# Optimization experiments

Hardware: AMD Instinct MI355X
Metric: run time of the kernel (lower is better)

## Reference

```python
import jax, jax.numpy as jnp
import numpy as np

N_NODES = 50000
N_EDGES = 640000
D_IN, D_HID, D_OUT = 128, 256, 2


def setup_inputs() -> dict:
    key = jax.random.key(0)
    ks = jax.random.split(key, 8)
    node_features = jax.random.normal(ks[0], (N_NODES, D_IN), dtype=jnp.float32)
    src = jax.random.randint(ks[1], (N_EDGES,), 0, N_NODES)
    dst = jax.random.randint(ks[2], (N_EDGES,), 0, N_NODES)
    s_in = 1.0 / np.sqrt(D_IN)
    s_hid = 1.0 / np.sqrt(D_HID)
    return {
        "node_features": node_features,
        "src": src,
        "dst": dst,
        "W1_self": jax.random.normal(ks[3], (D_IN, D_HID), dtype=jnp.float32) * s_in,
        "W1_neigh": jax.random.normal(ks[4], (D_IN, D_HID), dtype=jnp.float32) * s_in,
        "b1": jnp.zeros((D_HID,), dtype=jnp.float32),
        "W2_self": jax.random.normal(ks[5], (D_HID, D_OUT), dtype=jnp.float32) * s_hid,
        "W2_neigh": jax.random.normal(ks[6], (D_HID, D_OUT), dtype=jnp.float32) * s_hid,
        "b2": jnp.zeros((D_OUT,), dtype=jnp.float32),
    }


def _sage_mean(x, src, dst, W_self, W_neigh, b, n_nodes):
    # gather source-node features along edges, mean-reduce into destinations
    msg = x[src]                                                  # [E, D]
    agg = jax.ops.segment_sum(msg, dst, num_segments=n_nodes)     # [N, D]
    deg = jax.ops.segment_sum(jnp.ones((src.shape[0], 1), x.dtype), dst,
                              num_segments=n_nodes)               # [N, 1]
    h_neigh = agg / jnp.maximum(deg, 1.0)
    return x @ W_self + h_neigh @ W_neigh + b


def reference(node_features, src, dst, W1_self, W1_neigh, b1, W2_self, W2_neigh, b2):
    h = _sage_mean(node_features, src, dst, W1_self, W1_neigh, b1, N_NODES)
    h = jax.nn.relu(h)
    logits = _sage_mean(h, src, dst, W2_self, W2_neigh, b2, N_NODES)
    return logits
```

## Files before the change

### kernel.cpp

```cpp
#include <hip/hip_runtime.h>

#define D_IN 128
#define D_HID 256
#define CH 1024
#define MPAD 50048

typedef short bf16x8 __attribute__((ext_vector_type(8)));
typedef float f32x4 __attribute__((ext_vector_type(4)));
typedef float f32x16 __attribute__((ext_vector_type(16)));
typedef unsigned short ushort8 __attribute__((ext_vector_type(8)));

#define AS1 __attribute__((address_space(1)))
#define AS3 __attribute__((address_space(3)))

__device__ __forceinline__ unsigned short f2bf_rne(float x) {
  unsigned int u = __float_as_uint(x);
  unsigned int r = (u + 0x7FFFu + ((u >> 16) & 1u)) >> 16;
  return (unsigned short)r;
}
__device__ __forceinline__ float bf2f(unsigned short b) {
  return __uint_as_float(((unsigned int)b) << 16);
}

__global__ void k_hist(const int* __restrict__ dst, int* __restrict__ deg, int E) {
  int e = blockIdx.x * blockDim.x + threadIdx.x;
  if (e < E) atomicAdd(&deg[dst[e]], 1);
}

__global__ __launch_bounds__(256) void k_csum(const int* __restrict__ deg,
                                              int* __restrict__ csum, int n) {
  __shared__ int ws[4];
  int t = threadIdx.x, lane = t & 63, w = t >> 6;
  int base = blockIdx.x * CH + t * 4;
  int s = 0;
  #pragma unroll
  for (int j = 0; j < 4; ++j) { int i = base + j; s += (i < n) ? deg[i] : 0; }
  #pragma unroll
  for (int off = 32; off > 0; off >>= 1) s += __shfl_down(s, off, 64);
  if (lane == 0) ws[w] = s;
  __syncthreads();
  if (t == 0) csum[blockIdx.x] = ws[0] + ws[1] + ws[2] + ws[3];
}

__global__ void k_coff(const int* __restrict__ csum, int* __restrict__ coff, int nb) {
  int lane = threadIdx.x & 63;
  int v = (lane < nb) ? csum[lane] : 0;
  int x = v;
  #pragma unroll
  for (int off = 1; off < 64; off <<= 1) {
    int u = __shfl_up(x, off, 64);
    if (lane >= off) x += u;
  }
  if (lane < nb) coff[lane] = x - v;
}

__global__ __launch_bounds__(256) void k_scanw(const int* __restrict__ deg,
                                               const int* __restrict__ coff,
                                               int* __restrict__ rs, int n) {
  __shared__ int ws[4];
  int t = threadIdx.x, lane = t & 63, w = t >> 6;
  int base = blockIdx.x * CH + t * 4;
  int d[4];
  #pragma unroll
  for (int j = 0; j < 4; ++j) { int i = base + j; d[j] = (i < n) ? deg[i] : 0; }
  int tt = d[0] + d[1] + d[2] + d[3];
  int x = tt;
  #pragma unroll
  for (int off = 1; off < 64; off <<= 1) {
    int u = __shfl_up(x, off, 64);
    if (lane >= off) x += u;
  }
  if (lane == 63) ws[w] = x;
  __syncthreads();
  if (t == 0) { int s = 0;
    #pragma unroll
    for (int j = 0; j < 4; ++j) { int tmp = ws[j]; ws[j] = s; s += tmp; } }
  __syncthreads();
  int excl = ws[w] + (x - tt) + coff[blockIdx.x];
  #pragma unroll
  for (int j = 0; j < 4; ++j) {
    int i = base + j;
    excl += d[j];
    if (i < n) rs[i + 1] = excl;
  }
  if (blockIdx.x == 0 && t == 0) rs[0] = 0;
}

__global__ void k_scatter(const int* __restrict__ src, const int* __restrict__ dst,
                          const int* __restrict__ rs, int* __restrict__ cursor,
                          int* __restrict__ esrc, int E) {
  int e = blockIdx.x * blockDim.x + threadIdx.x;
  if (e < E) {
    int d = dst[e];
    int pos = rs[d] + atomicAdd(&cursor[d], 1);
    esrc[pos] = src[e];
  }
}

__global__ __launch_bounds__(256) void k_convW(const float* __restrict__ W1s,
                                               const float* __restrict__ W1n,
                                               unsigned short* __restrict__ Bth,
                                               unsigned short* __restrict__ Btl) {
  int k = blockIdx.x;
  int col = threadIdx.x;
  float w = (k < 128) ? W1s[(size_t)k * D_HID + col]
                      : W1n[(size_t)(k - 128) * D_HID + col];
  unsigned short hi = f2bf_rne(w);
  unsigned short lo = f2bf_rne(w - bf2f(hi));
  Bth[(size_t)col * 256 + k] = hi;
  Btl[(size_t)col * 256 + k] = lo;
}

__global__ void k_agg1(const float* __restrict__ X, const int* __restrict__ rs,
                       const int* __restrict__ esrc,
                       unsigned short* __restrict__ Mh,
                       unsigned short* __restrict__ Ml, int n) {
  int wid = (blockIdx.x * blockDim.x + threadIdx.x) >> 6;
  int lane = threadIdx.x & 63;
  if (wid >= n) return;
  int s0 = rs[wid], s1 = rs[wid + 1];
  float ax0 = 0.f, ay0 = 0.f, ax1 = 0.f, ay1 = 0.f;
  int e = s0;
  for (; e + 3 < s1; e += 4) {
    int i0 = esrc[e + 0], i1 = esrc[e + 1], i2 = esrc[e + 2], i3 = esrc[e + 3];
    float2 v0 = *(const float2*)(X + (size_t)i0 * D_IN + lane * 2);
    float2 v1 = *(const float2*)(X + (size_t)i1 * D_IN + lane * 2);
    float2 v2 = *(const float2*)(X + (size_t)i2 * D_IN + lane * 2);
    float2 v3 = *(const float2*)(X + (size_t)i3 * D_IN + lane * 2);
    ax0 += v0.x; ay0 += v0.y;
    ax1 += v1.x; ay1 += v1.y;
    ax0 += v2.x; ay0 += v2.y;
    ax1 += v3.x; ay1 += v3.y;
  }
  for (; e < s1; ++e) {
    int s = esrc[e];
    float2 v = *(const float2*)(X + (size_t)s * D_IN + lane * 2);
    ax0 += v.x; ay0 += v.y;
  }
  int d = s1 - s0;
  float inv = 1.0f / (float)(d > 1 ? d : 1);
  float mx = (ax0 + ax1) * inv, my = (ay0 + ay1) * inv;
  unsigned short hx = f2bf_rne(mx), hy = f2bf_rne(my);
  unsigned short lx = f2bf_rne(mx - bf2f(hx)), ly = f2bf_rne(my - bf2f(hy));
  *(ushort2*)(Mh + (size_t)wid * 128 + lane * 2) = make_ushort2(hx, hy);
  *(ushort2*)(Ml + (size_t)wid * 128 + lane * 2) = make_ushort2(lx, ly);
}

__global__ __launch_bounds__(256, 3) void k_gemm1(
    const float* __restrict__ X,
    const unsigned short* __restrict__ Mh, const unsigned short* __restrict__ Ml,
    const unsigned short* __restrict__ Bth, const unsigned short* __restrict__ Btl,
    const float* __restrict__ b1, const float* __restrict__ W2s,
    const float* __restrict__ W2n, float* __restrict__ SP, int n) {
  __shared__ __align__(16) unsigned short sA[2][2][2][512];
  __shared__ __align__(16) unsigned short sB[8][2][2][512];

  const int tid = threadIdx.x;
  const int w = tid >> 6;
  const int l = tid & 63;
  const int wm = w & 1, wn = w >> 1;
  const int r32 = l & 31;
  const int kh = l >> 5;
  const int m0 = blockIdx.x * 64;

  f32x16 acc[4];
  #pragma unroll
  for (int q = 0; q < 4; ++q) acc[q] = (f32x16)0.f;

  const int sm = w & 1, sk = w >> 1;
  const int arow = m0 + sm * 32 + r32;
  const int xrow = (arow < n) ? arow : (n - 1);

  for (int ks = 0; ks < 8; ++ks) {
    const int kt = ks * 32;
    if (kt < 128) {
      const float* src = X + (size_t)xrow * D_IN + kt + sk * 16 + kh * 8;
      float4 u0 = *(const float4*)(src);
      float4 u1 = *(const float4*)(src + 4);
      float v[8] = {u0.x, u0.y, u0.z, u0.w, u1.x, u1.y, u1.z, u1.w};
      ushort8 hh, ll;
      #pragma unroll
      for (int i = 0; i < 8; ++i) {
        unsigned short h = f2bf_rne(v[i]);
        hh[i] = h;
        ll[i] = f2bf_rne(v[i] - bf2f(h));
      }
      *(ushort8*)(&sA[sm][sk][0][l * 8]) = hh;
      *(ushort8*)(&sA[sm][sk][1][l * 8]) = ll;
    } else {
      const unsigned short* mh = Mh + (size_t)arow * 128 + (kt - 128) + sk * 16 + kh * 8;
      const unsigned short* ml = Ml + (size_t)arow * 128 + (kt - 128) + sk * 16 + kh * 8;
      __builtin_amdgcn_global_load_lds((AS1 const void*)mh, (AS3 void*)&sA[sm][sk][0][0], 16, 0, 0);
      __builtin_amdgcn_global_load_lds((AS1 const void*)ml, (AS3 void*)&sA[sm][sk][1][0], 16, 0, 0);
    }
    #pragma unroll
    for (int q = 0; q < 2; ++q) {
      int ct = w * 2 + q;
      #pragma unroll
      for (int kstep = 0; kstep < 2; ++kstep) {
        const unsigned short* bh = Bth + (size_t)(ct * 32 + r32) * 256 + kt + kstep * 16 + kh * 8;
        const unsigned short* bl = Btl + (size_t)(ct * 32 + r32) * 256 + kt + kstep * 16 + kh * 8;
        __builtin_amdgcn_global_load_lds((AS1 const void*)bh, (AS3 void*)&sB[ct][kstep][0][0], 16, 0, 0);
        __builtin_amdgcn_global_load_lds((AS1 const void*)bl, (AS3 void*)&sB[ct][kstep][1][0], 16, 0, 0);
      }
    }
    __syncthreads();

    #pragma unroll
    for (int kstep = 0; kstep < 2; ++kstep) {
      bf16x8 ah = *(const bf16x8*)(&sA[wm][kstep][0][l * 8]);
      bf16x8 al = *(const bf16x8*)(&sA[wm][kstep][1][l * 8]);
      #pragma unroll
      for (int q = 0; q < 4; ++q) {
        int ct = wn * 4 + q;
        bf16x8 bh = *(const bf16x8*)(&sB[ct][kstep][0][l * 8]);
        bf16x8 bl = *(const bf16x8*)(&sB[ct][kstep][1][l * 8]);
        acc[q] = __builtin_amdgcn_mfma_f32_32x32x16_bf16(ah, bh, acc[q], 0, 0, 0);
        acc[q] = __builtin_amdgcn_mfma_f32_32x32x16_bf16(ah, bl, acc[q], 0, 0, 0);
        acc[q] = __builtin_amdgcn_mfma_f32_32x32x16_bf16(al, bh, acc[q], 0, 0, 0);
      }
    }
    __syncthreads();
  }

  float b1v[4]; float2 w2sv[4], w2nv[4];
  #pragma unroll
  for (int q = 0; q < 4; ++q) {
    int col = wn * 128 + q * 32 + r32;
    b1v[q] = b1[col];
    w2sv[q] = *(const float2*)(W2s + (size_t)col * 2);
    w2nv[q] = *(const float2*)(W2n + (size_t)col * 2);
  }
  float4* fpart = (float4*)&sB[0][0][0][0];
  #pragma unroll
  for (int j = 0; j < 16; ++j) {
    float s0 = 0.f, s1 = 0.f, p0 = 0.f, p1 = 0.f;
    #pragma unroll
    for (int q = 0; q < 4; ++q) {
      float h = fmaxf(acc[q][j] + b1v[q], 0.f);
      s0 += h * w2sv[q].x; s1 += h * w2sv[q].y;
      p0 += h * w2nv[q].x; p1 += h * w2nv[q].y;
    }
    #pragma unroll
    for (int off = 1; off < 32; off <<= 1) {
      s0 += __shfl_xor(s0, off, 64);
      s1 += __shfl_xor(s1, off, 64);
      p0 += __shfl_xor(p0, off, 64);
      p1 += __shfl_xor(p1, off, 64);
    }
    if (r32 == 0) {
      int row = wm * 32 + (j & 3) + 8 * (j >> 2) + 4 * kh;
      float4 o; o.x = s0; o.y = s1; o.z = p0; o.w = p1;
      fpart[wn * 64 + row] = o;
    }
  }
  __syncthreads();
  if (w == 0) {
    float4 a = fpart[l], b = fpart[64 + l];
    float4 o; o.x = a.x + b.x; o.y = a.y + b.y; o.z = a.z + b.z; o.w = a.w + b.w;
    *(float4*)(SP + (size_t)(m0 + l) * 4) = o;
  }
}

__global__ void k_agg2(const float* __restrict__ SP,
                       const int* __restrict__ rs, const int* __restrict__ esrc,
                       const float* __restrict__ b2,
                       float* __restrict__ out, int n) {
  int nid = blockIdx.x * blockDim.x + threadIdx.x;
  if (nid >= n) return;
  int s0 = rs[nid], s1 = rs[nid + 1];
  float a00 = 0.f, a01 = 0.f, a10 = 0.f, a11 = 0.f;
  int e = s0;
  for (; e + 3 < s1; e += 4) {
    int i0 = esrc[e + 0], i1 = esrc[e + 1], i2 = esrc[e + 2], i3 = esrc[e + 3];
    float2 p0 = *(const float2*)(SP + (size_t)i0 * 4 + 2);
    float2 p1 = *(const float2*)(SP + (size_t)i1 * 4 + 2);
    float2 p2 = *(const float2*)(SP + (size_t)i2 * 4 + 2);
    float2 p3 = *(const float2*)(SP + (size_t)i3 * 4 + 2);
    a00 += p0.x; a01 += p0.y;
    a10 += p1.x; a11 += p1.y;
    a00 += p2.x; a01 += p2.y;
    a10 += p3.x; a11 += p3.y;
  }
  for (; e < s1; ++e) {
    int s = esrc[e];
    float2 p = *(const float2*)(SP + (size_t)s * 4 + 2);
    a00 += p.x; a01 += p.y;
  }
  int d = s1 - s0;
  float inv = 1.0f / (float)(d > 1 ? d : 1);
  float2 sv = *(const float2*)(SP + (size_t)nid * 4);
  float2 o;
  o.x = sv.x + b2[0] + (a00 + a10) * inv;
  o.y = sv.y + b2[1] + (a01 + a11) * inv;
  *(float2*)(out + (size_t)nid * 2) = o;
}

extern "C" void kernel_launch(void* const* d_in, const int* in_sizes, int n_in,
                              void* d_out, int out_size, void* d_ws, size_t ws_size,
                              hipStream_t stream) {
  const float* X   = (const float*)d_in[0];
  const int*   src = (const int*)d_in[1];
  const int*   dst = (const int*)d_in[2];
  const float* W1s = (const float*)d_in[3];
  const float* W1n = (const float*)d_in[4];
  const float* b1  = (const float*)d_in[5];
  const float* W2s = (const float*)d_in[6];
  const float* W2n = (const float*)d_in[7];
  const float* b2  = (const float*)d_in[8];
  float* out = (float*)d_out;

  const int N = in_sizes[0] / D_IN;
  const int E = in_sizes[1];
  const int NB = (N + CH - 1) / CH;

  int* deg    = (int*)d_ws;
  int* cursor = deg + N;
  int* rs     = cursor + N;
  int* csum   = rs + (N + 8);
  int* coff   = csum + 64;
  int* esrc   = coff + 64;
  float* SP   = (float*)(esrc + E);
  unsigned short* Mh  = (unsigned short*)(SP + (size_t)MPAD * 4);
  unsigned short* Ml  = Mh + (size_t)MPAD * 128;
  unsigned short* Bth = Ml + (size_t)MPAD * 128;
  unsigned short* Btl = Bth + 256 * 256;

  hipMemsetAsync(deg, 0, sizeof(int) * (size_t)2 * N, stream);

  int eb = (E + 255) / 256;
  k_convW  <<<256, 256, 0, stream>>>(W1s, W1n, Bth, Btl);
  k_hist   <<<eb, 256, 0, stream>>>(dst, deg, E);
  k_csum   <<<NB, 256, 0, stream>>>(deg, csum, N);
  k_coff   <<<1, 64, 0, stream>>>(csum, coff, NB);
  k_scanw  <<<NB, 256, 0, stream>>>(deg, coff, rs, N);
  k_scatter<<<eb, 256, 0, stream>>>(src, dst, rs, cursor, esrc, E);
  k_agg1   <<<(N + 3) / 4, 256, 0, stream>>>(X, rs, esrc, Mh, Ml, N);
  k_gemm1  <<<MPAD / 64, 256, 0, stream>>>(X, Mh, Ml, Bth, Btl,
                                           b1, W2s, W2n, SP, N);
  k_agg2   <<<(N + 255) / 256, 256, 0, stream>>>(SP, rs, esrc, b2, out, N);
}
```

Before: 255.7 us.

## Double-buffer LDS tiles in gemm1 to overlap loads with MFMA

Double-buffers the A and B shared-memory tiles in the fused layer-1 GEMM. The next k-slice is prefetched with global_load_lds while MFMAs run on the current buffer, and the loop drops from two barriers per iteration to one. The extra LDS doubles the footprint, so launch bounds fall from 3 to 2 blocks per CU, trading occupancy for overlap. The fp32 X rows are loaded into registers early and converted to bf16 hi/lo after the MFMAs.

```diff
diff --git a/kernel.cpp b/kernel.cpp
--- a/kernel.cpp
+++ b/kernel.cpp
@@ -146,14 +146,14 @@
   *(ushort2*)(Ml + (size_t)wid * 128 + lane * 2) = make_ushort2(lx, ly);
 }
 
-__global__ __launch_bounds__(256, 3) void k_gemm1(
+__global__ __launch_bounds__(256, 2) void k_gemm1(
     const float* __restrict__ X,
     const unsigned short* __restrict__ Mh, const unsigned short* __restrict__ Ml,
     const unsigned short* __restrict__ Bth, const unsigned short* __restrict__ Btl,
     const float* __restrict__ b1, const float* __restrict__ W2s,
     const float* __restrict__ W2n, float* __restrict__ SP, int n) {
-  __shared__ __align__(16) unsigned short sA[2][2][2][512];
-  __shared__ __align__(16) unsigned short sB[8][2][2][512];
+  __shared__ __align__(16) unsigned short sA[2][2][2][2][512];
+  __shared__ __align__(16) unsigned short sB[2][8][2][2][512];
 
   const int tid = threadIdx.x;
   const int w = tid >> 6;
@@ -171,13 +171,80 @@
   const int arow = m0 + sm * 32 + r32;
   const int xrow = (arow < n) ? arow : (n - 1);
 
+  {
+    const float* srcx = X + (size_t)xrow * D_IN + 0 + sk * 16 + kh * 8;
+    float4 u0 = *(const float4*)(srcx);
+    float4 u1 = *(const float4*)(srcx + 4);
+    float v[8] = {u0.x, u0.y, u0.z, u0.w, u1.x, u1.y, u1.z, u1.w};
+    ushort8 hh, ll;
+    #pragma unroll
+    for (int i = 0; i < 8; ++i) {
+      unsigned short h = f2bf_rne(v[i]);
+      hh[i] = h;
+      ll[i] = f2bf_rne(v[i] - bf2f(h));
+    }
+    *(ushort8*)(&sA[0][sm][sk][0][l * 8]) = hh;
+    *(ushort8*)(&sA[0][sm][sk][1][l * 8]) = ll;
+    #pragma unroll
+    for (int q = 0; q < 2; ++q) {
+      int ct = w * 2 + q;
+      #pragma unroll
+      for (int kstep = 0; kstep < 2; ++kstep) {
+        const unsigned short* bh = Bth + (size_t)(ct * 32 + r32) * 256 + 0 + kstep * 16 + kh * 8;
+        const unsigned short* bl = Btl + (size_t)(ct * 32 + r32) * 256 + 0 + kstep * 16 + kh * 8;
+        __builtin_amdgcn_global_load_lds((AS1 const void*)bh, (AS3 void*)&sB[0][ct][kstep][0][0], 16, 0, 0);
+        __builtin_amdgcn_global_load_lds((AS1 const void*)bl, (AS3 void*)&sB[0][ct][kstep][1][0], 16, 0, 0);
+      }
+    }
+  }
+  __syncthreads();
+
+  int cur = 0;
   for (int ks = 0; ks < 8; ++ks) {
-    const int kt = ks * 32;
-    if (kt < 128) {
-      const float* src = X + (size_t)xrow * D_IN + kt + sk * 16 + kh * 8;
-      float4 u0 = *(const float4*)(src);
-      float4 u1 = *(const float4*)(src + 4);
-      float v[8] = {u0.x, u0.y, u0.z, u0.w, u1.x, u1.y, u1.z, u1.w};
+    const int ktn = (ks + 1) * 32;
+    const int nxt = cur ^ 1;
+    float4 nu0, nu1;
+    bool nxtX = false;
+    if (ks < 7) {
+      if (ktn < 128) {
+        nxtX = true;
+        const float* srcx = X + (size_t)xrow * D_IN + ktn + sk * 16 + kh * 8;
+        nu0 = *(const float4*)(srcx);
+        nu1 = *(const float4*)(srcx + 4);
+      } else {
+        const unsigned short* mh = Mh + (size_t)arow * 128 + (ktn - 128) + sk * 16 + kh * 8;
+        const unsigned short* ml = Ml + (size_t)arow * 128 + (ktn - 128) + sk * 16 + kh * 8;
+        __builtin_amdgcn_global_load_lds((AS1 const void*)mh, (AS3 void*)&sA[nxt][sm][sk][0][0], 16, 0, 0);
+        __builtin_amdgcn_global_load_lds((AS1 const void*)ml, (AS3 void*)&sA[nxt][sm][sk][1][0], 16, 0, 0);
+      }
+      #pragma unroll
+      for (int q = 0; q < 2; ++q) {
+        int ct = w * 2 + q;
+        #pragma unroll
+        for (int kstep = 0; kstep < 2; ++kstep) {
+          const unsigned short* bh = Bth + (size_t)(ct * 32 + r32) * 256 + ktn + kstep * 16 + kh * 8;
+          const unsigned short* bl = Btl + (size_t)(ct * 32 + r32) * 256 + ktn + kstep * 16 + kh * 8;
+          __builtin_amdgcn_global_load_lds((AS1 const void*)bh, (AS3 void*)&sB[nxt][ct][kstep][0][0], 16, 0, 0);
+          __builtin_amdgcn_global_load_lds((AS1 const void*)bl, (AS3 void*)&sB[nxt][ct][kstep][1][0], 16, 0, 0);
+        }
+      }
+    }
+    #pragma unroll
+    for (int kstep = 0; kstep < 2; ++kstep) {
+      bf16x8 ah = *(const bf16x8*)(&sA[cur][wm][kstep][0][l * 8]);
+      bf16x8 al = *(const bf16x8*)(&sA[cur][wm][kstep][1][l * 8]);
+      #pragma unroll
+      for (int q = 0; q < 4; ++q) {
+        int ct = wn * 4 + q;
+        bf16x8 bh = *(const bf16x8*)(&sB[cur][ct][kstep][0][l * 8]);
+        bf16x8 bl = *(const bf16x8*)(&sB[cur][ct][kstep][1][l * 8]);
+        acc[q] = __builtin_amdgcn_mfma_f32_32x32x16_bf16(ah, bh, acc[q], 0, 0, 0);
+        acc[q] = __builtin_amdgcn_mfma_f32_32x32x16_bf16(ah, bl, acc[q], 0, 0, 0);
+        acc[q] = __builtin_amdgcn_mfma_f32_32x32x16_bf16(al, bh, acc[q], 0, 0, 0);
+      }
+    }
+    if (nxtX) {
+      float v[8] = {nu0.x, nu0.y, nu0.z, nu0.w, nu1.x, nu1.y, nu1.z, nu1.w};
       ushort8 hh, ll;
       #pragma unroll
       for (int i = 0; i < 8; ++i) {
@@ -185,42 +252,11 @@
         hh[i] = h;
         ll[i] = f2bf_rne(v[i] - bf2f(h));
       }
-      *(ushort8*)(&sA[sm][sk][0][l * 8]) = hh;
-      *(ushort8*)(&sA[sm][sk][1][l * 8]) = ll;
-    } else {
-      const unsigned short* mh = Mh + (size_t)arow * 128 + (kt - 128) + sk * 16 + kh * 8;
-      const unsigned short* ml = Ml + (size_t)arow * 128 + (kt - 128) + sk * 16 + kh * 8;
-      __builtin_amdgcn_global_load_lds((AS1 const void*)mh, (AS3 void*)&sA[sm][sk][0][0], 16, 0, 0);
-      __builtin_amdgcn_global_load_lds((AS1 const void*)ml, (AS3 void*)&sA[sm][sk][1][0], 16, 0, 0);
-    }
-    #pragma unroll
-    for (int q = 0; q < 2; ++q) {
-      int ct = w * 2 + q;
-      #pragma unroll
-      for (int kstep = 0; kstep < 2; ++kstep) {
-        const unsigned short* bh = Bth + (size_t)(ct * 32 + r32) * 256 + kt + kstep * 16 + kh * 8;
-        const unsigned short* bl = Btl + (size_t)(ct * 32 + r32) * 256 + kt + kstep * 16 + kh * 8;
-        __builtin_amdgcn_global_load_lds((AS1 const void*)bh, (AS3 void*)&sB[ct][kstep][0][0], 16, 0, 0);
-        __builtin_amdgcn_global_load_lds((AS1 const void*)bl, (AS3 void*)&sB[ct][kstep][1][0], 16, 0, 0);
-      }
+      *(ushort8*)(&sA[nxt][sm][sk][0][l * 8]) = hh;
+      *(ushort8*)(&sA[nxt][sm][sk][1][l * 8]) = ll;
     }
     __syncthreads();
-
-    #pragma unroll
-    for (int kstep = 0; kstep < 2; ++kstep) {
-      bf16x8 ah = *(const bf16x8*)(&sA[wm][kstep][0][l * 8]);
-      bf16x8 al = *(const bf16x8*)(&sA[wm][kstep][1][l * 8]);
-      #pragma unroll
-      for (int q = 0; q < 4; ++q) {
-        int ct = wn * 4 + q;
-        bf16x8 bh = *(const bf16x8*)(&sB[ct][kstep][0][l * 8]);
-        bf16x8 bl = *(const bf16x8*)(&sB[ct][kstep][1][l * 8]);
-        acc[q] = __builtin_amdgcn_mfma_f32_32x32x16_bf16(ah, bh, acc[q], 0, 0, 0);
-        acc[q] = __builtin_amdgcn_mfma_f32_32x32x16_bf16(ah, bl, acc[q], 0, 0, 0);
-        acc[q] = __builtin_amdgcn_mfma_f32_32x32x16_bf16(al, bh, acc[q], 0, 0, 0);
-      }
-    }
-    __syncthreads();
+    cur ^= 1;
   }
 
   float b1v[4]; float2 w2sv[4], w2nv[4];
@@ -231,7 +267,7 @@
     w2sv[q] = *(const float2*)(W2s + (size_t)col * 2);
     w2nv[q] = *(const float2*)(W2n + (size_t)col * 2);
   }
-  float4* fpart = (float4*)&sB[0][0][0][0];
+  float4* fpart = (float4*)&sB[0][0][0][0][0];
   #pragma unroll
   for (int j = 0; j < 16; ++j) {
     float s0 = 0.f, s1 = 0.f, p0 = 0.f, p1 = 0.f;
```

Result: slower. 267.6 us (+4.6%).

## Drop LDS staging in gemm1; load fragments directly from global memory

Applied to the files above, without the earlier changes.

Rewrites the layer-1 GEMM so that each wave loads its A (X converted to split bf16, plus the aggregated means) and B fragments straight from global memory into registers, with no shared-memory staging and no per-k-step barriers. The warp tiling changes from a 2x2 layout (32 rows by 128 columns per wave) to each wave owning all 64 rows and a 64-column slice. The fused ReLU/W2 epilogue now reduces partials across four waves instead of two. This removes LDS traffic and syncthreads, but every wave redundantly loads and converts the same A rows. The launch-bounds occupancy hint also drops from 3 to 2 blocks per CU.

```diff
diff --git a/kernel.cpp b/kernel.cpp
--- a/kernel.cpp
+++ b/kernel.cpp
@@ -8,10 +8,6 @@
 typedef short bf16x8 __attribute__((ext_vector_type(8)));
 typedef float f32x4 __attribute__((ext_vector_type(4)));
 typedef float f32x16 __attribute__((ext_vector_type(16)));
-typedef unsigned short ushort8 __attribute__((ext_vector_type(8)));
-
-#define AS1 __attribute__((address_space(1)))
-#define AS3 __attribute__((address_space(3)))
 
 __device__ __forceinline__ unsigned short f2bf_rne(float x) {
   unsigned int u = __float_as_uint(x);
@@ -146,119 +142,147 @@
   *(ushort2*)(Ml + (size_t)wid * 128 + lane * 2) = make_ushort2(lx, ly);
 }
 
-__global__ __launch_bounds__(256, 3) void k_gemm1(
+__global__ __launch_bounds__(256, 2) void k_gemm1(
     const float* __restrict__ X,
     const unsigned short* __restrict__ Mh, const unsigned short* __restrict__ Ml,
     const unsigned short* __restrict__ Bth, const unsigned short* __restrict__ Btl,
     const float* __restrict__ b1, const float* __restrict__ W2s,
     const float* __restrict__ W2n, float* __restrict__ SP, int n) {
-  __shared__ __align__(16) unsigned short sA[2][2][2][512];
-  __shared__ __align__(16) unsigned short sB[8][2][2][512];
+  __shared__ float4 part[4][64];
 
   const int tid = threadIdx.x;
   const int w = tid >> 6;
   const int l = tid & 63;
-  const int wm = w & 1, wn = w >> 1;
   const int r32 = l & 31;
   const int kh = l >> 5;
+  const int kh8 = kh * 8;
   const int m0 = blockIdx.x * 64;
-
-  f32x16 acc[4];
-  #pragma unroll
-  for (int q = 0; q < 4; ++q) acc[q] = (f32x16)0.f;
-
-  const int sm = w & 1, sk = w >> 1;
-  const int arow = m0 + sm * 32 + r32;
-  const int xrow = (arow < n) ? arow : (n - 1);
-
-  for (int ks = 0; ks < 8; ++ks) {
-    const int kt = ks * 32;
-    if (kt < 128) {
-      const float* src = X + (size_t)xrow * D_IN + kt + sk * 16 + kh * 8;
-      float4 u0 = *(const float4*)(src);
-      float4 u1 = *(const float4*)(src + 4);
-      float v[8] = {u0.x, u0.y, u0.z, u0.w, u1.x, u1.y, u1.z, u1.w};
-      ushort8 hh, ll;
+  const int c0 = w * 64;
+
+  f32x16 acc[2][2];
+  #pragma unroll
+  for (int rt = 0; rt < 2; ++rt)
+    #pragma unroll
+    for (int ct = 0; ct < 2; ++ct) acc[rt][ct] = (f32x16)0.f;
+
+  int xr0 = m0 + r32;       if (xr0 >= n) xr0 = n - 1;
+  int xr1 = m0 + 32 + r32;  if (xr1 >= n) xr1 = n - 1;
+  const int mr0 = m0 + r32, mr1 = m0 + 32 + r32;
+
+  #pragma unroll
+  for (int ksc = 0; ksc < 4; ++ksc) {
+    #pragma unroll
+    for (int ks2 = 0; ks2 < 2; ++ks2) {
+      const int ko = ksc * 32 + ks2 * 16 + kh8;
+      bf16x8 ah[2], al[2];
+      const float* sx0 = X + (size_t)xr0 * D_IN + ko;
+      const float* sx1 = X + (size_t)xr1 * D_IN + ko;
+      float4 a0 = *(const float4*)sx0, a1 = *(const float4*)(sx0 + 4);
+      float4 b0 = *(const float4*)sx1, b1q = *(const float4*)(sx1 + 4);
+      {
+        float v[8] = {a0.x, a0.y, a0.z, a0.w, a1.x, a1.y, a1.z, a1.w};
+        bf16x8 hh, ll;
+        #pragma unroll
+        for (int i = 0; i < 8; ++i) {
+          unsigned short h = f2bf_rne(v[i]);
+          hh[i] = (short)h;
+          ll[i] = (short)f2bf_rne(v[i] - bf2f(h));
+        }
+        ah[0] = hh; al[0] = ll;
+      }
+      {
+        float v[8] = {b0.x, b0.y, b0.z, b0.w, b1q.x, b1q.y, b1q.z, b1q.w};
+        bf16x8 hh, ll;
+        #pragma unroll
+        for (int i = 0; i < 8; ++i) {
+          unsigned short h = f2bf_rne(v[i]);
+          hh[i] = (short)h;
+          ll[i] = (short)f2bf_rne(v[i] - bf2f(h));
+        }
+        ah[1] = hh; al[1] = ll;
+      }
       #pragma unroll
-      for (int i = 0; i < 8; ++i) {
-        unsigned short h = f2bf_rne(v[i]);
-        hh[i] = h;
-        ll[i] = f2bf_rne(v[i] - bf2f(h));
-      }
-      *(ushort8*)(&sA[sm][sk][0][l * 8]) = hh;
-      *(ushort8*)(&sA[sm][sk][1][l * 8]) = ll;
-    } else {
-      const unsigned short* mh = Mh + (size_t)arow * 128 + (kt - 128) + sk * 16 + kh * 8;
-      const unsigned short* ml = Ml + (size_t)arow * 128 + (kt - 128) + sk * 16 + kh * 8;
-      __builtin_amdgcn_global_load_lds((AS1 const void*)mh, (AS3 void*)&sA[sm][sk][0][0], 16, 0, 0);
-      __builtin_amdgcn_global_load_lds((AS1 const void*)ml, (AS3 void*)&sA[sm][sk][1][0], 16, 0, 0);
+      for (int ct = 0; ct < 2; ++ct) {
+        const size_t boff = (size_t)(c0 + ct * 32 + r32) * 256 + ko;
+        bf16x8 bh = *(const bf16x8*)(Bth + boff);
+        bf16x8 bl = *(const bf16x8*)(Btl + boff);
+        #pragma unroll
+        for (int rt = 0; rt < 2; ++rt) {
+          acc[rt][ct] = __builtin_amdgcn_mfma_f32_32x32x16_bf16(ah[rt], bh, acc[rt][ct], 0, 0, 0);
+          acc[rt][ct] = __builtin_amdgcn_mfma_f32_32x32x16_bf16(ah[rt], bl, acc[rt][ct], 0, 0, 0);
+          acc[rt][ct] = __builtin_amdgcn_mfma_f32_32x32x16_bf16(al[rt], bh, acc[rt][ct], 0, 0, 0);
+        }
+      }
     }
-    #pragma unroll
-    for (int q = 0; q < 2; ++q) {
-      int ct = w * 2 + q;
+  }
+  #pragma unroll
+  for (int ksc = 0; ksc < 4; ++ksc) {
+    #pragma unroll
+    for (int ks2 = 0; ks2 < 2; ++ks2) {
+      const int km = ksc * 32 + ks2 * 16 + kh8;
+      const int ko = 128 + km;
+      bf16x8 ah[2], al[2];
+      ah[0] = *(const bf16x8*)(Mh + (size_t)mr0 * 128 + km);
+      al[0] = *(const bf16x8*)(Ml + (size_t)mr0 * 128 + km);
+      ah[1] = *(const bf16x8*)(Mh + (size_t)mr1 * 128 + km);
+      al[1] = *(const bf16x8*)(Ml + (size_t)mr1 * 128 + km);
       #pragma unroll
-      for (int kstep = 0; kstep < 2; ++kstep) {
-        const unsigned short* bh = Bth + (size_t)(ct * 32 + r32) * 256 + kt + kstep * 16 + kh * 8;
-        const unsigned short* bl = Btl + (size_t)(ct * 32 + r32) * 256 + kt + kstep * 16 + kh * 8;
-        __builtin_amdgcn_global_load_lds((AS1 const void*)bh, (AS3 void*)&sB[ct][kstep][0][0], 16, 0, 0);
-        __builtin_amdgcn_global_load_lds((AS1 const void*)bl, (AS3 void*)&sB[ct][kstep][1][0], 16, 0, 0);
+      for (int ct = 0; ct < 2; ++ct) {
+        const size_t boff = (size_t)(c0 + ct * 32 + r32) * 256 + ko;
+        bf16x8 bh = *(const bf16x8*)(Bth + boff);
+        bf16x8 bl = *(const bf16x8*)(Btl + boff);
+        #pragma unroll
+        for (int rt = 0; rt < 2; ++rt) {
+          acc[rt][ct] = __builtin_amdgcn_mfma_f32_32x32x16_bf16(ah[rt], bh, acc[rt][ct], 0, 0, 0);
+          acc[rt][ct] = __builtin_amdgcn_mfma_f32_32x32x16_bf16(ah[rt], bl, acc[rt][ct], 0, 0, 0);
+          acc[rt][ct] = __builtin_amdgcn_mfma_f32_32x32x16_bf16(al[rt], bh, acc[rt][ct], 0, 0, 0);
+        }
       }
     }
-    __syncthreads();
-
-    #pragma unroll
-    for (int kstep = 0; kstep < 2; ++kstep) {
-      bf16x8 ah = *(const bf16x8*)(&sA[wm][kstep][0][l * 8]);
-      bf16x8 al = *(const bf16x8*)(&sA[wm][kstep][1][l * 8]);
+  }
+
+  float b1v[2]; float2 w2sv[2], w2nv[2];
+  #pragma unroll
+  for (int ct = 0; ct < 2; ++ct) {
+    int col = c0 + ct * 32 + r32;
+    b1v[ct] = b1[col];
+    w2sv[ct] = *(const float2*)(W2s + (size_t)col * 2);
+    w2nv[ct] = *(const float2*)(W2n + (size_t)col * 2);
+  }
+  #pragma unroll
+  for (int rt = 0; rt < 2; ++rt) {
+    #pragma unroll
+    for (int j = 0; j < 16; ++j) {
+      float s0 = 0.f, s1 = 0.f, p0 = 0.f, p1 = 0.f;
       #pragma unroll
-      for (int q = 0; q < 4; ++q) {
-        int ct = wn * 4 + q;
-        bf16x8 bh = *(const bf16x8*)(&sB[ct][kstep][0][l * 8]);
-        bf16x8 bl = *(const bf16x8*)(&sB[ct][kstep][1][l * 8]);
-        acc[q] = __builtin_amdgcn_mfma_f32_32x32x16_bf16(ah, bh, acc[q], 0, 0, 0);
-        acc[q] = __builtin_amdgcn_mfma_f32_32x32x16_bf16(ah, bl, acc[q], 0, 0, 0);
-        acc[q] = __builtin_amdgcn_mfma_f32_32x32x16_bf16(al, bh, acc[q], 0, 0, 0);
+      for (int ct = 0; ct < 2; ++ct) {
+        float h = fmaxf(acc[rt][ct][j] + b1v[ct], 0.f);
+        s0 += h * w2sv[ct].x; s1 += h * w2sv[ct].y;
+        p0 += h * w2nv[ct].x; p1 += h * w2nv[ct].y;
+      }
+      #pragma unroll
+      for (int off = 1; off < 32; off <<= 1) {
+        s0 += __shfl_xor(s0, off, 64);
+        s1 += __shfl_xor(s1, off, 64);
+        p0 += __shfl_xor(p0, off, 64);
+        p1 += __shfl_xor(p1, off, 64);
+      }
+      if (r32 == 0) {
+        int row = rt * 32 + (j & 3) + 8 * (j >> 2) + 4 * kh;
+        float4 o; o.x = s0; o.y = s1; o.z = p0; o.w = p1;
+        part[w][row] = o;
       }
     }
-    __syncthreads();
-  }
-
-  float b1v[4]; float2 w2sv[4], w2nv[4];
-  #pragma unroll
-  for (int q = 0; q < 4; ++q) {
-    int col = wn * 128 + q * 32 + r32;
-    b1v[q] = b1[col];
-    w2sv[q] = *(const float2*)(W2s + (size_t)col * 2);
-    w2nv[q] = *(const float2*)(W2n + (size_t)col * 2);
-  }
-  float4* fpart = (float4*)&sB[0][0][0][0];
-  #pragma unroll
-  for (int j = 0; j < 16; ++j) {
-    float s0 = 0.f, s1 = 0.f, p0 = 0.f, p1 = 0.f;
-    #pragma unroll
-    for (int q = 0; q < 4; ++q) {
-      float h = fmaxf(acc[q][j] + b1v[q], 0.f);
-      s0 += h * w2sv[q].x; s1 += h * w2sv[q].y;
-      p0 += h * w2nv[q].x; p1 += h * w2nv[q].y;
-    }
-    #pragma unroll
-    for (int off = 1; off < 32; off <<= 1) {
-      s0 += __shfl_xor(s0, off, 64);
-      s1 += __shfl_xor(s1, off, 64);
-      p0 += __shfl_xor(p0, off, 64);
-      p1 += __shfl_xor(p1, off, 64);
-    }
-    if (r32 == 0) {
-      int row = wm * 32 + (j & 3) + 8 * (j >> 2) + 4 * kh;
-      float4 o; o.x = s0; o.y = s1; o.z = p0; o.w = p1;
-      fpart[wn * 64 + row] = o;
-    }
   }
   __syncthreads();
-  if (w == 0) {
-    float4 a = fpart[l], b = fpart[64 + l];
-    float4 o; o.x = a.x + b.x; o.y = a.y + b.y; o.z = a.z + b.z; o.w = a.w + b.w;
-    *(float4*)(SP + (size_t)(m0 + l) * 4) = o;
+  if (tid < 64) {
+    float4 a = part[0][tid], b = part[1][tid], c = part[2][tid], d = part[3][tid];
+    float4 o;
+    o.x = (a.x + b.x) + (c.x + d.x);
+    o.y = (a.y + b.y) + (c.y + d.y);
+    o.z = (a.z + b.z) + (c.z + d.z);
+    o.w = (a.w + b.w) + (c.w + d.w);
+    *(float4*)(SP + (size_t)(m0 + tid) * 4) = o;
   }
 }
 
```

After: 276.5 us. 8.1% more time.

## Split gemm1 output columns across two blocks with atomic partial reduction

Applied to the files above, without the earlier changes.

The fused layer-1 GEMM now launches a 2D grid in which each block computes 128 of the 256 hidden columns. The per-row layer-2 projections are combined across the two column halves with float atomicAdd into a zeroed SP buffer. This halves per-block shared memory and accumulator registers, raises launch bounds to 4 blocks per CU and doubles block count, aiming for more occupancy and parallelism. The cost is that the A-side loads and fp32 to bf16 conversion of X are done twice, plus an extra memset and atomic traffic.

```diff
diff --git a/kernel.cpp b/kernel.cpp
--- a/kernel.cpp
+++ b/kernel.cpp
@@ -146,14 +146,15 @@
   *(ushort2*)(Ml + (size_t)wid * 128 + lane * 2) = make_ushort2(lx, ly);
 }
 
-__global__ __launch_bounds__(256, 3) void k_gemm1(
+__global__ __launch_bounds__(256, 4) void k_gemm1(
     const float* __restrict__ X,
     const unsigned short* __restrict__ Mh, const unsigned short* __restrict__ Ml,
     const unsigned short* __restrict__ Bth, const unsigned short* __restrict__ Btl,
     const float* __restrict__ b1, const float* __restrict__ W2s,
     const float* __restrict__ W2n, float* __restrict__ SP, int n) {
   __shared__ __align__(16) unsigned short sA[2][2][2][512];
-  __shared__ __align__(16) unsigned short sB[8][2][2][512];
+  __shared__ __align__(16) unsigned short sB[4][2][2][512];
+  __shared__ float4 part[2][64];
 
   const int tid = threadIdx.x;
   const int w = tid >> 6;
@@ -161,11 +162,12 @@
   const int wm = w & 1, wn = w >> 1;
   const int r32 = l & 31;
   const int kh = l >> 5;
+  const int kh8 = kh * 8;
   const int m0 = blockIdx.x * 64;
-
-  f32x16 acc[4];
-  #pragma unroll
-  for (int q = 0; q < 4; ++q) acc[q] = (f32x16)0.f;
+  const int c0 = blockIdx.y * 128;
+
+  f32x16 acc[2];
+  acc[0] = (f32x16)0.f; acc[1] = (f32x16)0.f;
 
   const int sm = w & 1, sk = w >> 1;
   const int arow = m0 + sm * 32 + r32;
@@ -174,9 +176,9 @@
   for (int ks = 0; ks < 8; ++ks) {
     const int kt = ks * 32;
     if (kt < 128) {
-      const float* src = X + (size_t)xrow * D_IN + kt + sk * 16 + kh * 8;
-      float4 u0 = *(const float4*)(src);
-      float4 u1 = *(const float4*)(src + 4);
+      const float* srcx = X + (size_t)xrow * D_IN + kt + sk * 16 + kh8;
+      float4 u0 = *(const float4*)(srcx);
+      float4 u1 = *(const float4*)(srcx + 4);
       float v[8] = {u0.x, u0.y, u0.z, u0.w, u1.x, u1.y, u1.z, u1.w};
       ushort8 hh, ll;
       #pragma unroll
@@ -188,21 +190,17 @@
       *(ushort8*)(&sA[sm][sk][0][l * 8]) = hh;
       *(ushort8*)(&sA[sm][sk][1][l * 8]) = ll;
     } else {
-      const unsigned short* mh = Mh + (size_t)arow * 128 + (kt - 128) + sk * 16 + kh * 8;
-      const unsigned short* ml = Ml + (size_t)arow * 128 + (kt - 128) + sk * 16 + kh * 8;
+      const unsigned short* mh = Mh + (size_t)arow * 128 + (kt - 128) + sk * 16 + kh8;
+      const unsigned short* ml = Ml + (size_t)arow * 128 + (kt - 128) + sk * 16 + kh8;
       __builtin_amdgcn_global_load_lds((AS1 const void*)mh, (AS3 void*)&sA[sm][sk][0][0], 16, 0, 0);
       __builtin_amdgcn_global_load_lds((AS1 const void*)ml, (AS3 void*)&sA[sm][sk][1][0], 16, 0, 0);
     }
     #pragma unroll
-    for (int q = 0; q < 2; ++q) {
-      int ct = w * 2 + q;
-      #pragma unroll
-      for (int kstep = 0; kstep < 2; ++kstep) {
-        const unsigned short* bh = Bth + (size_t)(ct * 32 + r32) * 256 + kt + kstep * 16 + kh * 8;
-        const unsigned short* bl = Btl + (size_t)(ct * 32 + r32) * 256 + kt + kstep * 16 + kh * 8;
-        __builtin_amdgcn_global_load_lds((AS1 const void*)bh, (AS3 void*)&sB[ct][kstep][0][0], 16, 0, 0);
-        __builtin_amdgcn_global_load_lds((AS1 const void*)bl, (AS3 void*)&sB[ct][kstep][1][0], 16, 0, 0);
-      }
+    for (int kstep = 0; kstep < 2; ++kstep) {
+      const unsigned short* bh = Bth + (size_t)(c0 + w * 32 + r32) * 256 + kt + kstep * 16 + kh8;
+      const unsigned short* bl = Btl + (size_t)(c0 + w * 32 + r32) * 256 + kt + kstep * 16 + kh8;
+      __builtin_amdgcn_global_load_lds((AS1 const void*)bh, (AS3 void*)&sB[w][kstep][0][0], 16, 0, 0);
+      __builtin_amdgcn_global_load_lds((AS1 const void*)bl, (AS3 void*)&sB[w][kstep][1][0], 16, 0, 0);
     }
     __syncthreads();
 
@@ -211,8 +209,8 @@
       bf16x8 ah = *(const bf16x8*)(&sA[wm][kstep][0][l * 8]);
       bf16x8 al = *(const bf16x8*)(&sA[wm][kstep][1][l * 8]);
       #pragma unroll
-      for (int q = 0; q < 4; ++q) {
-        int ct = wn * 4 + q;
+      for (int q = 0; q < 2; ++q) {
+        int ct = wn * 2 + q;
         bf16x8 bh = *(const bf16x8*)(&sB[ct][kstep][0][l * 8]);
         bf16x8 bl = *(const bf16x8*)(&sB[ct][kstep][1][l * 8]);
         acc[q] = __builtin_amdgcn_mfma_f32_32x32x16_bf16(ah, bh, acc[q], 0, 0, 0);
@@ -223,20 +221,19 @@
     __syncthreads();
   }
 
-  float b1v[4]; float2 w2sv[4], w2nv[4];
-  #pragma unroll
-  for (int q = 0; q < 4; ++q) {
-    int col = wn * 128 + q * 32 + r32;
+  float b1v[2]; float2 w2sv[2], w2nv[2];
+  #pragma unroll
+  for (int q = 0; q < 2; ++q) {
+    int col = c0 + (wn * 2 + q) * 32 + r32;
     b1v[q] = b1[col];
     w2sv[q] = *(const float2*)(W2s + (size_t)col * 2);
     w2nv[q] = *(const float2*)(W2n + (size_t)col * 2);
   }
-  float4* fpart = (float4*)&sB[0][0][0][0];
   #pragma unroll
   for (int j = 0; j < 16; ++j) {
     float s0 = 0.f, s1 = 0.f, p0 = 0.f, p1 = 0.f;
     #pragma unroll
-    for (int q = 0; q < 4; ++q) {
+    for (int q = 0; q < 2; ++q) {
       float h = fmaxf(acc[q][j] + b1v[q], 0.f);
       s0 += h * w2sv[q].x; s1 += h * w2sv[q].y;
       p0 += h * w2nv[q].x; p1 += h * w2nv[q].y;
@@ -251,14 +248,17 @@
     if (r32 == 0) {
       int row = wm * 32 + (j & 3) + 8 * (j >> 2) + 4 * kh;
       float4 o; o.x = s0; o.y = s1; o.z = p0; o.w = p1;
-      fpart[wn * 64 + row] = o;
+      part[wn][row] = o;
     }
   }
   __syncthreads();
-  if (w == 0) {
-    float4 a = fpart[l], b = fpart[64 + l];
-    float4 o; o.x = a.x + b.x; o.y = a.y + b.y; o.z = a.z + b.z; o.w = a.w + b.w;
-    *(float4*)(SP + (size_t)(m0 + l) * 4) = o;
+  if (tid < 64) {
+    float4 a = part[0][tid], b = part[1][tid];
+    float* sp = SP + (size_t)(m0 + tid) * 4;
+    atomicAdd(sp + 0, a.x + b.x);
+    atomicAdd(sp + 1, a.y + b.y);
+    atomicAdd(sp + 2, a.z + b.z);
+    atomicAdd(sp + 3, a.w + b.w);
   }
 }
 
@@ -327,6 +327,7 @@
   unsigned short* Btl = Bth + 256 * 256;
 
   hipMemsetAsync(deg, 0, sizeof(int) * (size_t)2 * N, stream);
+  hipMemsetAsync(SP, 0, sizeof(float) * (size_t)MPAD * 4, stream);
 
   int eb = (E + 255) / 256;
   k_convW  <<<256, 256, 0, stream>>>(W1s, W1n, Bth, Btl);
@@ -336,7 +337,7 @@
   k_scanw  <<<NB, 256, 0, stream>>>(deg, coff, rs, N);
   k_scatter<<<eb, 256, 0, stream>>>(src, dst, rs, cursor, esrc, E);
   k_agg1   <<<(N + 3) / 4, 256, 0, stream>>>(X, rs, esrc, Mh, Ml, N);
-  k_gemm1  <<<MPAD / 64, 256, 0, stream>>>(X, Mh, Ml, Bth, Btl,
-                                           b1, W2s, W2n, SP, N);
+  k_gemm1  <<<dim3(MPAD / 64, 2), 256, 0, stream>>>(X, Mh, Ml, Bth, Btl,
+                                                    b1, W2s, W2n, SP, N);
   k_agg2   <<<(N + 255) / 256, 256, 0, stream>>>(SP, rs, esrc, b2, out, N);
 }
```

Measured after the change: 264.9 us. +3.6%, slower.
